# Performance work log

Hardware: AMD Instinct MI355X
Metric: run time of the kernel (lower is better)

Reference implementation:

```python
import jax, jax.numpy as jnp
import numpy as np

N_BINS = 15


def setup_inputs() -> dict:
    key = jax.random.key(0)
    k1, k2 = jax.random.split(key)
    N, C = 65536, 1000
    logits = jax.random.normal(k1, (N, C), dtype=jnp.float32)
    labels = jax.random.randint(k2, (N,), 0, C, dtype=jnp.int64)
    return {"logits": logits, "labels": labels}


def reference(logits, labels):
    # softmax confidences, per-class correctness indicators
    N, C = logits.shape
    conf = jax.nn.softmax(logits, axis=1)                       # [N, C]
    acc = (jnp.arange(C)[None, :] == labels[:, None]).astype(conf.dtype)  # [N, C]

    # Bin assignment replicating (conf > lower) & (conf <= upper) with
    # boundaries linspace(0,1,n_bins+1): bin b covers (b/n_bins, (b+1)/n_bins].
    # conf == 0 falls in no bin -> route to dummy segment N_BINS.
    bin_idx = jnp.clip(jnp.ceil(conf * N_BINS).astype(jnp.int32) - 1, 0, N_BINS - 1)
    bin_idx = jnp.where(conf > 0.0, bin_idx, N_BINS)            # [N, C]
    col_idx = jnp.broadcast_to(jnp.arange(C, dtype=jnp.int32), (N, C))

    # Fused per-(bin, class) histogram scatter: counts, sum conf, sum acc.
    zeros = jnp.zeros((N_BINS + 1, C), dtype=conf.dtype)
    counts = zeros.at[bin_idx, col_idx].add(1.0)[:N_BINS]        # [B, C]
    sum_conf = zeros.at[bin_idx, col_idx].add(conf)[:N_BINS]     # [B, C]
    sum_acc = zeros.at[bin_idx, col_idx].add(acc)[:N_BINS]       # [B, C]

    prob_in_bin = counts / N
    safe = jnp.maximum(counts, 1.0)
    avg_conf = sum_conf / safe
    avg_acc = sum_acc / safe
    per_bin = jnp.where(counts > 0, jnp.abs(avg_conf - avg_acc) * prob_in_bin, 0.0)
    ece = jnp.sum(per_bin) / C
    return ece.reshape(1)
```

## Files before the change

### kernel.cpp

```cpp
#include <hip/hip_runtime.h>
#include <hip/hip_bf16.h>
#include <math.h>

#define NBINS   15
#define CDIM    1000
#define QDIM    250
#define HIST_ELEMS (NBINS * CDIM)
#define THREADS 512
#define NWAVES  (THREADS / 64)
#define PAD     -1000.0f

__device__ __forceinline__ float waveSum(float v) {
#pragma unroll
    for (int o = 32; o > 0; o >>= 1) v += __shfl_xor(v, o, 64);
    return v;
}

__device__ __forceinline__ void loadRow(float4 (&v)[4], int& label,
                                        const float* __restrict__ logits,
                                        const int* __restrict__ labels,
                                        int r, int lane) {
    const float4* row = (const float4*)(logits + (size_t)r * CDIM);
#pragma unroll
    for (int j = 0; j < 4; ++j) {
        int q = lane + 64 * j;
        v[j] = (q < QDIM) ? row[q] : make_float4(PAD, PAD, PAD, PAD);
    }
    label = labels[r];
}

__device__ __forceinline__ void computeRow(float4 (&v)[4], int label, int lane,
                                           float (&regAcc)[4][4],
                                           float* __restrict__ D) {
    float s = 0.0f;
#pragma unroll
    for (int j = 0; j < 4; ++j) {
        v[j].x = __expf(v[j].x);
        v[j].y = __expf(v[j].y);
        v[j].z = __expf(v[j].z);
        v[j].w = __expf(v[j].w);
        s += (v[j].x + v[j].y) + (v[j].z + v[j].w);
    }
    s = waveSum(s);
    const float inv = 1.0f / s;

#pragma unroll
    for (int j = 0; j < 4; ++j) {
        const int q = lane + 64 * j;
        const float cf[4] = {v[j].x, v[j].y, v[j].z, v[j].w};
#pragma unroll
        for (int k = 0; k < 4; ++k) {
            float conf = cf[k] * inv;
            float t    = conf * 15.0f;
            float add  = conf - ((4 * q + k == label) ? 1.0f : 0.0f);
            if (t > 1.0f) {
                int b = min((int)ceilf(t) - 1, NBINS - 1);
                unsafeAtomicAdd(&D[b * CDIM + k * QDIM + q], add);
            } else {
                regAcc[j][k] += add;
            }
        }
    }
}

__global__ __launch_bounds__(THREADS, 4) void ece_hist_kernel(
        const float* __restrict__ logits,
        const int*   __restrict__ labels,
        float*       __restrict__ D,
        int N, int rowsPerBlock)
{
    __shared__ float sB[CDIM];

    const int tid  = threadIdx.x;
    const int lane = tid & 63;
    const int w    = tid >> 6;

    for (int i = tid; i < CDIM; i += THREADS) sB[i] = 0.0f;
    __syncthreads();

    const int r0 = blockIdx.x * rowsPerBlock;
    const int r1 = min(r0 + rowsPerBlock, N);

    float regAcc[4][4];
#pragma unroll
    for (int j = 0; j < 4; ++j)
#pragma unroll
        for (int k = 0; k < 4; ++k) regAcc[j][k] = 0.0f;

    float4 vA[4], vB[4], vC[4];
    int    lA = 0, lB = 0, lC = 0;

    int rA = r0 + w;
    int rB = rA + NWAVES;
    int rC = rB + NWAVES;

    if (rA < r1) loadRow(vA, lA, logits, labels, rA, lane);
    if (rB < r1) loadRow(vB, lB, logits, labels, rB, lane);
    if (rC < r1) loadRow(vC, lC, logits, labels, rC, lane);

    while (rA < r1) {
        computeRow(vA, lA, lane, regAcc, D);
        rA = rC + NWAVES;
        if (rA < r1) loadRow(vA, lA, logits, labels, rA, lane);

        if (rB >= r1) break;
        computeRow(vB, lB, lane, regAcc, D);
        rB = rA + NWAVES;
        if (rB < r1) loadRow(vB, lB, logits, labels, rB, lane);

        if (rC >= r1) break;
        computeRow(vC, lC, lane, regAcc, D);
        rC = rB + NWAVES;
        if (rC < r1) loadRow(vC, lC, logits, labels, rC, lane);
    }

#pragma unroll
    for (int j = 0; j < 4; ++j) {
        int q = lane + 64 * j;
        if (q < QDIM) {
#pragma unroll
            for (int k = 0; k < 4; ++k)
                unsafeAtomicAdd(&sB[k * QDIM + q], regAcc[j][k]);
        }
    }

    __syncthreads();
    for (int i = tid; i < CDIM; i += THREADS) {
        float val = sB[i];
        if (val != 0.0f) unsafeAtomicAdd(&D[i], val);
    }
}

__global__ __launch_bounds__(1024) void ece_final_kernel(
        const float* __restrict__ D, float* __restrict__ out, float scale)
{
    float s = 0.0f;
    for (int i = threadIdx.x; i < HIST_ELEMS; i += 1024)
        s += fabsf(D[i]);
    s = waveSum(s);
    __shared__ float sr[16];
    const int lane = threadIdx.x & 63;
    const int wid  = threadIdx.x >> 6;
    if (lane == 0) sr[wid] = s;
    __syncthreads();
    if (threadIdx.x == 0) {
        float t = 0.0f;
#pragma unroll
        for (int ww = 0; ww < 16; ++ww) t += sr[ww];
        out[0] = t * scale;
    }
}

extern "C" void kernel_launch(void* const* d_in, const int* in_sizes, int n_in,
                              void* d_out, int out_size, void* d_ws, size_t ws_size,
                              hipStream_t stream)
{
    const float* logits = (const float*)d_in[0];
    const int*   labels = (const int*)d_in[1];

    const int N = in_sizes[1];

    float* D = (float*)d_ws;
    hipMemsetAsync(D, 0, HIST_ELEMS * sizeof(float), stream);

    const int grid = 512;
    const int rowsPerBlock = (N + grid - 1) / grid;

    ece_hist_kernel<<<grid, THREADS, 0, stream>>>(logits, labels, D, N, rowsPerBlock);

    const float scale = 1.0f / ((float)N * (float)CDIM);
    ece_final_kernel<<<1, 1024, 0, stream>>>(D, (float*)d_out, scale);
}
```

Measured before the change: 83.48 us.

## Add wave-uniform fast path for rows with no high-confidence entries

Computes the row max alongside the exp sum and, when no element in the wave exceeds the first bin boundary, accumulates confidences into registers with plain FMAs instead of per-element compare and branch logic. The label correction is now handled separately by a single owning lane via readfirstlane. The change also deepens the row prefetch from three to four rows, simplifies the row load, and vectorizes the final reduction with float4 loads. This trades extra register pressure from the fourth row buffer and extra label-selection logic for fewer per-element branches.

```diff
diff --git a/kernel.cpp b/kernel.cpp
--- a/kernel.cpp
+++ b/kernel.cpp
@@ -1,5 +1,4 @@
 #include <hip/hip_runtime.h>
-#include <hip/hip_bf16.h>
 #include <math.h>
 
 #define NBINS   15
@@ -9,6 +8,7 @@
 #define THREADS 512
 #define NWAVES  (THREADS / 64)
 #define PAD     -1000.0f
+#define RARE_LIM (1.0f)
 
 __device__ __forceinline__ float waveSum(float v) {
 #pragma unroll
@@ -22,17 +22,16 @@
                                         int r, int lane) {
     const float4* row = (const float4*)(logits + (size_t)r * CDIM);
 #pragma unroll
-    for (int j = 0; j < 4; ++j) {
-        int q = lane + 64 * j;
-        v[j] = (q < QDIM) ? row[q] : make_float4(PAD, PAD, PAD, PAD);
-    }
+    for (int j = 0; j < 3; ++j) v[j] = row[lane + 64 * j];
+    v[3] = make_float4(PAD, PAD, PAD, PAD);
+    if (lane < QDIM - 192) v[3] = row[lane + 192];
     label = labels[r];
 }
 
 __device__ __forceinline__ void computeRow(float4 (&v)[4], int label, int lane,
                                            float (&regAcc)[4][4],
                                            float* __restrict__ D) {
-    float s = 0.0f;
+    float s = 0.0f, m = 0.0f;
 #pragma unroll
     for (int j = 0; j < 4; ++j) {
         v[j].x = __expf(v[j].x);
@@ -40,26 +39,69 @@
         v[j].z = __expf(v[j].z);
         v[j].w = __expf(v[j].w);
         s += (v[j].x + v[j].y) + (v[j].z + v[j].w);
+        m = fmaxf(m, fmaxf(fmaxf(v[j].x, v[j].y), fmaxf(v[j].z, v[j].w)));
     }
     s = waveSum(s);
     const float inv = 1.0f / s;
 
-#pragma unroll
-    for (int j = 0; j < 4; ++j) {
-        const int q = lane + 64 * j;
-        const float cf[4] = {v[j].x, v[j].y, v[j].z, v[j].w};
-#pragma unroll
-        for (int k = 0; k < 4; ++k) {
-            float conf = cf[k] * inv;
-            float t    = conf * 15.0f;
-            float add  = conf - ((4 * q + k == label) ? 1.0f : 0.0f);
-            if (t > 1.0f) {
-                int b = min((int)ceilf(t) - 1, NBINS - 1);
-                unsafeAtomicAdd(&D[b * CDIM + k * QDIM + q], add);
-            } else {
-                regAcc[j][k] += add;
+    const bool rare = __any((m * inv) * 15.0f > RARE_LIM);
+
+    if (!rare) {
+#pragma unroll
+        for (int j = 0; j < 4; ++j) {
+            regAcc[j][0] = fmaf(v[j].x, inv, regAcc[j][0]);
+            regAcc[j][1] = fmaf(v[j].y, inv, regAcc[j][1]);
+            regAcc[j][2] = fmaf(v[j].z, inv, regAcc[j][2]);
+            regAcc[j][3] = fmaf(v[j].w, inv, regAcc[j][3]);
+        }
+    } else {
+#pragma unroll
+        for (int j = 0; j < 4; ++j) {
+            const int q = lane + 64 * j;
+            const float cf[4] = {v[j].x, v[j].y, v[j].z, v[j].w};
+#pragma unroll
+            for (int k = 0; k < 4; ++k) {
+                float conf = cf[k] * inv;
+                float t    = conf * 15.0f;
+                if (t > RARE_LIM) {
+                    int b = min((int)ceilf(t) - 1, NBINS - 1);
+                    unsafeAtomicAdd(&D[b * CDIM + k * QDIM + q], conf);
+                } else {
+                    regAcc[j][k] += conf;
+                }
             }
         }
+    }
+
+    const int sl    = __builtin_amdgcn_readfirstlane(label);
+    const int lq    = sl >> 2;
+    const int lk    = sl & 3;
+    const int lj    = lq >> 6;
+    const int llane = lq & 63;
+
+    float cfl;
+    if      (lj == 0) cfl = (lk == 0) ? v[0].x : (lk == 1) ? v[0].y : (lk == 2) ? v[0].z : v[0].w;
+    else if (lj == 1) cfl = (lk == 0) ? v[1].x : (lk == 1) ? v[1].y : (lk == 2) ? v[1].z : v[1].w;
+    else if (lj == 2) cfl = (lk == 0) ? v[2].x : (lk == 1) ? v[2].y : (lk == 2) ? v[2].z : v[2].w;
+    else              cfl = (lk == 0) ? v[3].x : (lk == 1) ? v[3].y : (lk == 2) ? v[3].z : v[3].w;
+
+    const float confl = cfl * inv;
+    const bool  own   = (lane == llane);
+
+    if (own && confl * 15.0f > RARE_LIM) {
+        int b = min((int)ceilf(confl * 15.0f) - 1, NBINS - 1);
+        unsafeAtomicAdd(&D[b * CDIM + lk * QDIM + lq], -1.0f);
+    } else {
+        const float dec = own ? 1.0f : 0.0f;
+#define LBL_CASE(J)                                                         \
+        if (lj == J) {                                                      \
+            if      (lk == 0) regAcc[J][0] -= dec;                          \
+            else if (lk == 1) regAcc[J][1] -= dec;                          \
+            else if (lk == 2) regAcc[J][2] -= dec;                          \
+            else              regAcc[J][3] -= dec;                          \
+        }
+        LBL_CASE(0) else LBL_CASE(1) else LBL_CASE(2) else LBL_CASE(3)
+#undef LBL_CASE
     }
 }
 
@@ -87,20 +129,22 @@
 #pragma unroll
         for (int k = 0; k < 4; ++k) regAcc[j][k] = 0.0f;
 
-    float4 vA[4], vB[4], vC[4];
-    int    lA = 0, lB = 0, lC = 0;
+    float4 vA[4], vB[4], vC[4], vD2[4];
+    int    lA = 0, lB = 0, lC = 0, lD = 0;
 
     int rA = r0 + w;
     int rB = rA + NWAVES;
     int rC = rB + NWAVES;
-
-    if (rA < r1) loadRow(vA, lA, logits, labels, rA, lane);
-    if (rB < r1) loadRow(vB, lB, logits, labels, rB, lane);
-    if (rC < r1) loadRow(vC, lC, logits, labels, rC, lane);
+    int rD = rC + NWAVES;
+
+    if (rA < r1) loadRow(vA,  lA, logits, labels, rA, lane);
+    if (rB < r1) loadRow(vB,  lB, logits, labels, rB, lane);
+    if (rC < r1) loadRow(vC,  lC, logits, labels, rC, lane);
+    if (rD < r1) loadRow(vD2, lD, logits, labels, rD, lane);
 
     while (rA < r1) {
         computeRow(vA, lA, lane, regAcc, D);
-        rA = rC + NWAVES;
+        rA = rD + NWAVES;
         if (rA < r1) loadRow(vA, lA, logits, labels, rA, lane);
 
         if (rB >= r1) break;
@@ -112,6 +156,11 @@
         computeRow(vC, lC, lane, regAcc, D);
         rC = rB + NWAVES;
         if (rC < r1) loadRow(vC, lC, logits, labels, rC, lane);
+
+        if (rD >= r1) break;
+        computeRow(vD2, lD, lane, regAcc, D);
+        rD = rC + NWAVES;
+        if (rD < r1) loadRow(vD2, lD, logits, labels, rD, lane);
     }
 
 #pragma unroll
@@ -135,8 +184,11 @@
         const float* __restrict__ D, float* __restrict__ out, float scale)
 {
     float s = 0.0f;
-    for (int i = threadIdx.x; i < HIST_ELEMS; i += 1024)
-        s += fabsf(D[i]);
+    const float4* D4 = (const float4*)D;
+    for (int i = threadIdx.x; i < HIST_ELEMS / 4; i += 1024) {
+        float4 t = D4[i];
+        s += (fabsf(t.x) + fabsf(t.y)) + (fabsf(t.z) + fabsf(t.w));
+    }
     s = waveSum(s);
     __shared__ float sr[16];
     const int lane = threadIdx.x & 63;
```

Result: slower. 180.5 us (+116.3%).
